# Performance work log

Measured on AMD Instinct MI355X. Metric: run time of the kernel, lower is better.

## Reference

```python
import jax, jax.numpy as jnp
import numpy as np

N_NODES = 100000
N_EDGES = 3200000
DIM = 128
N_LAYERS = 3
NUM_GRAPHS = 128
BN_EPS = 1e-5
GIN_EPS = 0.0  # eps buffer initialized to 0, train_eps=False


def setup_inputs() -> dict:
    key = jax.random.key(0)
    ks = jax.random.split(key, 12)
    s = 1.0 / np.sqrt(DIM)
    inp = {
        "x": jax.random.normal(ks[0], (N_NODES, DIM), jnp.float32),
        "edge_index": jax.random.randint(ks[1], (2, N_EDGES), 0, N_NODES, jnp.int64),
        "batch": jnp.sort(jax.random.randint(ks[2], (N_NODES,), 0, NUM_GRAPHS, jnp.int64)),
        # node encoder Linear(x_dim, emb_dim)
        "W_node": jax.random.uniform(ks[3], (DIM, DIM), jnp.float32, -s, s),
        "b_node": jax.random.uniform(ks[4], (DIM,), jnp.float32, -s, s),
        # per-layer MLP: Linear -> BatchNorm -> ReLU -> Linear, stacked over layers
        "W1": jax.random.uniform(ks[5], (N_LAYERS, DIM, DIM), jnp.float32, -s, s),
        "b1": jax.random.uniform(ks[6], (N_LAYERS, DIM), jnp.float32, -s, s),
        "gamma": jnp.ones((N_LAYERS, DIM), jnp.float32),
        "beta": jnp.zeros((N_LAYERS, DIM), jnp.float32),
        "W2": jax.random.uniform(ks[7], (N_LAYERS, DIM, DIM), jnp.float32, -s, s),
        "b2": jax.random.uniform(ks[8], (N_LAYERS, DIM), jnp.float32, -s, s),
    }
    return inp


def _batchnorm(y, gamma, beta):
    # training-mode batch statistics over the node dimension (biased variance)
    mean = jnp.mean(y, axis=0)
    var = jnp.mean(jnp.square(y - mean), axis=0)
    return (y - mean) * jax.lax.rsqrt(var + BN_EPS) * gamma + beta


def reference(x, edge_index, batch, W_node, b_node, W1, b1, gamma, beta, W2, b2):
    src, dst = edge_index[0], edge_index[1]
    n = x.shape[0]
    h = x @ W_node + b_node  # [N, D]
    for i in range(N_LAYERS):
        # GINConv: scatter-add gathered neighbor features, eps-residual, MLP
        agg = jax.ops.segment_sum(h[src], dst, num_segments=n)  # [N, D]
        out = agg + (1.0 + GIN_EPS) * h
        y = out @ W1[i] + b1[i]
        y = jax.nn.relu(_batchnorm(y, gamma[i], beta[i]))
        y = y @ W2[i] + b2[i]
        h = jax.nn.relu(y)  # outer ReLU in Encoder.forward (dropout_p=0)
    # global_add_pool
    return jax.ops.segment_sum(h, batch, num_segments=NUM_GRAPHS)  # [G, D]
```

## Files before the change

### kernel.cpp

```cpp
#include <hip/hip_runtime.h>

#define N_NODES 100000
#define M_PAD   100096
#define N_EDGES 3200000
#define DIM 128
#define N_LAYERS 3
#define NUM_GRAPHS 128
#define BN_EPS 1e-5f

#define DST_SHIFT 7
#define BUCKET_NODES 128
#define N_BUCKETS ((N_NODES + BUCKET_NODES - 1) / BUCKET_NODES)
#define BUCKET_CAP 4864
#define EDGES_PER_BLOCK 16384
#define BIN_BLOCKS ((N_EDGES + EDGES_PER_BLOCK - 1) / EDGES_PER_BLOCK)
#define N_BANDS 64

typedef unsigned int uint32;
typedef unsigned short u16;
typedef __attribute__((ext_vector_type(8))) short bf16x8;
typedef __attribute__((ext_vector_type(4))) float f32x4;

__device__ __forceinline__ float bf2f(u16 u) {
    union { uint32 i; float f; } c;
    c.i = ((uint32)u) << 16;
    return c.f;
}
__device__ __forceinline__ u16 f2bf(float f) {
    union { float f; uint32 i; } c;
    c.f = f;
    uint32 i = c.i;
    return (u16)((i + 0x7FFFu + ((i >> 16) & 1u)) >> 16);
}
__device__ __forceinline__ float lo_bf(uint32 v) {
    union { uint32 i; float f; } c;
    c.i = v << 16;
    return c.f;
}
__device__ __forceinline__ float hi_bf(uint32 v) {
    union { uint32 i; float f; } c;
    c.i = v & 0xFFFF0000u;
    return c.f;
}
__device__ __forceinline__ uint32 pack_bf2(float a, float b) {
    return ((uint32)f2bf(b) << 16) | (uint32)f2bf(a);
}
__device__ __forceinline__ void unpack_add8(float* acc, uint4 v) {
    acc[0] += lo_bf(v.x); acc[1] += hi_bf(v.x);
    acc[2] += lo_bf(v.y); acc[3] += hi_bf(v.y);
    acc[4] += lo_bf(v.z); acc[5] += hi_bf(v.z);
    acc[6] += lo_bf(v.w); acc[7] += hi_bf(v.w);
}

__global__ __launch_bounds__(256) void zero_misc(int* __restrict__ gcur,
                                                 float* __restrict__ bn_stats,
                                                 float* __restrict__ outp,
                                                 uint32* __restrict__ aggpad32) {
    int i = blockIdx.x * 256 + threadIdx.x;
    if (i < N_BUCKETS) gcur[i] = 0;
    if (i < N_LAYERS * 2 * DIM) bn_stats[i] = 0.f;
    if (i < NUM_GRAPHS * DIM) outp[i] = 0.f;
    if (i < (M_PAD - N_NODES) * DIM / 2) aggpad32[i] = 0;
}

__global__ __launch_bounds__(256) void bin_by_dst(const int* __restrict__ src,
                                                  const int* __restrict__ dst,
                                                  int* __restrict__ gcur,
                                                  uint32* __restrict__ packed) {
    __shared__ int cnt[N_BUCKETS];
    __shared__ int cur[N_BUCKETS];
    int t = threadIdx.x;
    int e0 = blockIdx.x * EDGES_PER_BLOCK;
    for (int i = t; i < N_BUCKETS; i += 256) cnt[i] = 0;
    __syncthreads();

    for (int j = 0; j < EDGES_PER_BLOCK / 256; ++j) {
        int e = e0 + j * 256 + t;
        if (e < N_EDGES) atomicAdd(&cnt[dst[e] >> DST_SHIFT], 1);
    }
    __syncthreads();
    for (int i = t; i < N_BUCKETS; i += 256) {
        int c = cnt[i];
        cur[i] = c ? atomicAdd(&gcur[i], c) : 0;
    }
    __syncthreads();
    for (int j = 0; j < EDGES_PER_BLOCK / 256; ++j) {
        int e = e0 + j * 256 + t;
        if (e < N_EDGES) {
            int d = dst[e];
            int b = d >> DST_SHIFT;
            int pos = atomicAdd(&cur[b], 1);
            if (pos < BUCKET_CAP)
                packed[(size_t)b * BUCKET_CAP + pos] =
                    (uint32)src[e] | ((uint32)(d & (BUCKET_NODES - 1)) << 17);
        }
    }
}

__global__ void scan_buckets(const int* __restrict__ gcur, int* __restrict__ obase,
                             int* __restrict__ row_ptr) {
    __shared__ int s[N_BUCKETS];
    int t = threadIdx.x;
    for (int i = t; i < N_BUCKETS; i += 256) {
        int c = gcur[i];
        s[i] = (c > BUCKET_CAP) ? BUCKET_CAP : c;
    }
    __syncthreads();
    if (t == 0) {
        int run = 0;
        for (int i = 0; i < N_BUCKETS; ++i) {
            int c = s[i];
            s[i] = run;
            run += c;
        }
        row_ptr[N_NODES] = run;
    }
    __syncthreads();
    for (int i = t; i < N_BUCKETS; i += 256) obase[i] = s[i];
}

__global__ __launch_bounds__(256) void build_buckets(const uint32* __restrict__ packed,
                                                     const int* __restrict__ gcur,
                                                     const int* __restrict__ obase_arr,
                                                     int* __restrict__ row_ptr,
                                                     int* __restrict__ col_src) {
    __shared__ uint32 ed[BUCKET_CAP];
    __shared__ uint32 ed2[BUCKET_CAP];
    __shared__ int bandcur[N_BANDS];
    __shared__ int ncnt[BUCKET_NODES];
    __shared__ int ncur[BUCKET_NODES];
    int b = blockIdx.x, t = threadIdx.x;
    int cnt = gcur[b];
    if (cnt > BUCKET_CAP) cnt = BUCKET_CAP;
    int obase = obase_arr[b];
    int n0 = b * BUCKET_NODES;

    if (t < N_BANDS) bandcur[t] = 0;
    if (t < BUCKET_NODES) ncnt[t] = 0;
    __syncthreads();

    const uint32* reg = packed + (size_t)b * BUCKET_CAP;
    for (int i = t; i < cnt; i += 256) {
        uint32 v = reg[i];
        ed[i] = v;
        atomicAdd(&bandcur[(v & 0x1FFFFu) >> 11], 1);
        atomicAdd(&ncnt[v >> 17], 1);
    }
    __syncthreads();

    if (t == 0) {
        int run = 0;
        for (int w = 0; w < N_BANDS; ++w) {
            int c = bandcur[w];
            bandcur[w] = run;
            run += c;
        }
    }
    int myc = (t < BUCKET_NODES) ? ncnt[t] : 0;
    if (t < BUCKET_NODES) ncur[t] = myc;
    __syncthreads();
    for (int off = 1; off < BUCKET_NODES; off <<= 1) {
        int v = 0;
        if (t < BUCKET_NODES && t >= off) v = ncur[t - off];
        __syncthreads();
        if (t < BUCKET_NODES) ncur[t] += v;
        __syncthreads();
    }
    if (t < BUCKET_NODES) {
        int excl = ncur[t] - myc;
        ncur[t] = excl;
        int gn = n0 + t;
        if (gn < N_NODES) row_ptr[gn] = obase + excl;
    }
    __syncthreads();

    for (int i = t; i < cnt; i += 256) {
        uint32 v = ed[i];
        int p = atomicAdd(&bandcur[(v & 0x1FFFFu) >> 11], 1);
        ed2[p] = v;
    }
    __syncthreads();

    for (int i = t; i < cnt; i += 256) {
        uint32 v = ed2[i];
        int slot = atomicAdd(&ncur[v >> 17], 1);
        col_src[obase + slot] = (int)(v & 0x1FFFFu);
    }
}

__global__ void cvt_wt_all(const float* __restrict__ Wn, const float* __restrict__ W1,
                           const float* __restrict__ W2, u16* __restrict__ WT) {
    int m = blockIdx.x >> 7, n = blockIdx.x & 127, k = threadIdx.x;
    const float* src = (m == 0) ? Wn
                     : (m <= 3) ? W1 + (size_t)(m - 1) * DIM * DIM
                                : W2 + (size_t)(m - 4) * DIM * DIM;
    int L = n * 256 + k * 2;
    int Ls = L ^ ((n & 7) << 4);
    *(u16*)((char*)WT + (size_t)m * 32768 + Ls) = f2bf(src[(size_t)k * DIM + n]);
}

__global__ __launch_bounds__(256) void aggregate_bf(const u16* __restrict__ h,
                                                    const int* __restrict__ row_ptr,
                                                    const int* __restrict__ col_src,
                                                    u16* __restrict__ agg) {
    int t = threadIdx.x;
    int quad = (blockIdx.x * 256 + t) >> 4;
    int c = t & 15;
    int nA = quad * 2;
    if (nA >= N_NODES) return;
    int nB = nA + 1;
    const uint4* h4 = (const uint4*)h;

    int begA = row_ptr[nA], endA = row_ptr[nA + 1];
    int begB = row_ptr[nB], endB = row_ptr[nB + 1];
    int lenA = endA - begA, lenB = endB - begB;
    int m = lenA < lenB ? lenA : lenB;

    float a_[8], b_[8];
#pragma unroll
    for (int j = 0; j < 8; ++j) { a_[j] = 0.f; b_[j] = 0.f; }

    {
        uint4 sA = h4[(size_t)nA * 16 + c];
        uint4 sB = h4[(size_t)nB * 16 + c];
        unpack_add8(a_, sA);
        unpack_add8(b_, sB);
    }

    int i = 0;
    for (; i + 2 <= m; i += 2) {
        int iA0 = col_src[begA + i], iA1 = col_src[begA + i + 1];
        int iB0 = col_src[begB + i], iB1 = col_src[begB + i + 1];
        uint4 vA0 = h4[(size_t)iA0 * 16 + c];
        uint4 vB0 = h4[(size_t)iB0 * 16 + c];
        uint4 vA1 = h4[(size_t)iA1 * 16 + c];
        uint4 vB1 = h4[(size_t)iB1 * 16 + c];
        unpack_add8(a_, vA0);
        unpack_add8(b_, vB0);
        unpack_add8(a_, vA1);
        unpack_add8(b_, vB1);
    }
    if (i < m) {
        uint4 vA = h4[(size_t)col_src[begA + i] * 16 + c];
        uint4 vB = h4[(size_t)col_src[begB + i] * 16 + c];
        unpack_add8(a_, vA);
        unpack_add8(b_, vB);
        ++i;
    }
    for (int e = begA + i; e < endA; ++e) {
        uint4 v = h4[(size_t)col_src[e] * 16 + c];
        unpack_add8(a_, v);
    }
    for (int e = begB + i; e < endB; ++e) {
        uint4 v = h4[(size_t)col_src[e] * 16 + c];
        unpack_add8(b_, v);
    }

    uint4 oA, oB;
    oA.x = pack_bf2(a_[0], a_[1]); oA.y = pack_bf2(a_[2], a_[3]);
    oA.z = pack_bf2(a_[4], a_[5]); oA.w = pack_bf2(a_[6], a_[7]);
    oB.x = pack_bf2(b_[0], b_[1]); oB.y = pack_bf2(b_[2], b_[3]);
    oB.z = pack_bf2(b_[4], b_[5]); oB.w = pack_bf2(b_[6], b_[7]);
    *(uint4*)&agg[(size_t)nA * DIM + c * 8] = oA;
    *(uint4*)&agg[(size_t)nB * DIM + c * 8] = oB;
}

template <int MODE>
__global__ __launch_bounds__(256) void gemm_v2(const void* __restrict__ Av,
                                               const u16* __restrict__ WTs,
                                               const float* __restrict__ bias,
                                               u16* __restrict__ outp,
                                               float* __restrict__ bn_sum,
                                               float* __restrict__ bn_sumsq,
                                               const float* __restrict__ gamma,
                                               const float* __restrict__ beta) {
    __shared__ u16 sB[DIM * DIM];
    __shared__ float sc_[DIM];
    __shared__ float sh_[DIM];
    __shared__ float ls[4][DIM];
    __shared__ float lq[4][DIM];

    int t = threadIdx.x;
    int wid = t >> 6, lane = t & 63;
    int hw = lane >> 4, c = lane & 15;
    int row0 = blockIdx.x * 128 + wid * 32;

    bf16x8 a[2][4];
    float4 af[2][4][2];
#pragma unroll
    for (int rf = 0; rf < 2; ++rf) {
        int row = row0 + rf * 16 + c;
#pragma unroll
        for (int ks = 0; ks < 4; ++ks) {
            int k0 = ks * 32 + hw * 8;
            if (MODE == 0) {
                const float* xf = (const float*)Av;
                af[rf][ks][0] = make_float4(0.f, 0.f, 0.f, 0.f);
                af[rf][ks][1] = af[rf][ks][0];
                if (row < N_NODES) {
                    af[rf][ks][0] = *(const float4*)&xf[(size_t)row * DIM + k0];
                    af[rf][ks][1] = *(const float4*)&xf[(size_t)row * DIM + k0 + 4];
                }
            } else {
                const u16* Ab = (const u16*)Av;
                a[rf][ks] = *(const bf16x8*)&Ab[(size_t)row * DIM + k0];
            }
        }
    }

    {
        const uint4* Wg = (const uint4*)WTs;
        uint4* sB4 = (uint4*)sB;
#pragma unroll
        for (int i = 0; i < 8; ++i) sB4[i * 256 + t] = Wg[i * 256 + t];
    }
    if (MODE == 2 && t < DIM) {
        const float invN = 1.0f / (float)N_NODES;
        float mean = bn_sum[t] * invN;
        float var = fmaxf(bn_sumsq[t] * invN - mean * mean, 0.f);
        float rs = rsqrtf(var + BN_EPS);
        float sc = gamma[t] * rs;
        sc_[t] = sc;
        sh_[t] = beta[t] - mean * sc;
    }
    __syncthreads();

#pragma unroll
    for (int rf = 0; rf < 2; ++rf) {
#pragma unroll
        for (int ks = 0; ks < 4; ++ks) {
            int k0 = ks * 32 + hw * 8;
            if (MODE == 0) {
                union { bf16x8 v; u16 u[8]; } ua;
                float4 v0 = af[rf][ks][0], v1 = af[rf][ks][1];
                ua.u[0] = f2bf(v0.x); ua.u[1] = f2bf(v0.y);
                ua.u[2] = f2bf(v0.z); ua.u[3] = f2bf(v0.w);
                ua.u[4] = f2bf(v1.x); ua.u[5] = f2bf(v1.y);
                ua.u[6] = f2bf(v1.z); ua.u[7] = f2bf(v1.w);
                a[rf][ks] = ua.v;
            } else if (MODE == 2) {
                union { bf16x8 v; u16 u[8]; } ua;
                ua.v = a[rf][ks];
#pragma unroll
                for (int j = 0; j < 8; ++j) {
                    float f = bf2f(ua.u[j]);
                    f = fmaxf(fmaf(f, sc_[k0 + j], sh_[k0 + j]), 0.f);
                    ua.u[j] = f2bf(f);
                }
                a[rf][ks] = ua.v;
            }
        }
    }

    f32x4 acc[2][8];
#pragma unroll
    for (int rf = 0; rf < 2; ++rf)
#pragma unroll
        for (int nf = 0; nf < 8; ++nf) acc[rf][nf] = (f32x4){0.f, 0.f, 0.f, 0.f};

    int swz = (c & 7) << 4;
#pragma unroll
    for (int ks = 0; ks < 4; ++ks) {
#pragma unroll
        for (int nf = 0; nf < 8; ++nf) {
            int L = (nf * 4096 + c * 256 + ks * 64 + hw * 16) ^ swz;
            bf16x8 b = *(const bf16x8*)((const char*)sB + L);
            acc[0][nf] = __builtin_amdgcn_mfma_f32_16x16x32_bf16(a[0][ks], b, acc[0][nf], 0, 0, 0);
            acc[1][nf] = __builtin_amdgcn_mfma_f32_16x16x32_bf16(a[1][ks], b, acc[1][nf], 0, 0, 0);
        }
    }

    float s_[8], q_[8];
#pragma unroll
    for (int nf = 0; nf < 8; ++nf) { s_[nf] = 0.f; q_[nf] = 0.f; }

#pragma unroll
    for (int rf = 0; rf < 2; ++rf) {
        int rbase = row0 + rf * 16 + hw * 4;
#pragma unroll
        for (int nf = 0; nf < 8; ++nf) {
            float bv = bias[nf * 16 + c];
#pragma unroll
            for (int r = 0; r < 4; ++r) {
                float v = acc[rf][nf][r] + bv;
                if (MODE == 2) v = fmaxf(v, 0.f);
                outp[(size_t)(rbase + r) * DIM + nf * 16 + c] = f2bf(v);
                if (MODE == 1) {
                    float m = (rbase + r < N_NODES) ? v : 0.f;
                    s_[nf] += m;
                    q_[nf] += m * m;
                }
            }
        }
    }

    if (MODE == 1) {
#pragma unroll
        for (int nf = 0; nf < 8; ++nf) {
            s_[nf] += __shfl_xor(s_[nf], 16);
            s_[nf] += __shfl_xor(s_[nf], 32);
            q_[nf] += __shfl_xor(q_[nf], 16);
            q_[nf] += __shfl_xor(q_[nf], 32);
        }
        if (lane < 16) {
#pragma unroll
            for (int nf = 0; nf < 8; ++nf) {
                ls[wid][nf * 16 + c] = s_[nf];
                lq[wid][nf * 16 + c] = q_[nf];
            }
        }
        __syncthreads();
        if (t < DIM) {
            atomicAdd(&bn_sum[t], ls[0][t] + ls[1][t] + ls[2][t] + ls[3][t]);
            atomicAdd(&bn_sumsq[t], lq[0][t] + lq[1][t] + lq[2][t] + lq[3][t]);
        }
    }
}

__global__ __launch_bounds__(256) void pool_bf(const u16* __restrict__ h,
                                               const int* __restrict__ batch,
                                               float* __restrict__ out) {
    int wv = (blockIdx.x * 256 + threadIdx.x) >> 6;
    int lane = threadIdx.x & 63;
    int base = wv * 32;
    if (base >= N_NODES) return;
    int end = base + 32;
    if (end > N_NODES) end = N_NODES;
    const uint32* h32 = (const uint32*)h;
    float ax = 0.f, ay = 0.f;
    int curg = batch[base];
    for (int n = base; n < end; ++n) {
        int g = batch[n];
        if (g != curg) {
            atomicAdd(&out[curg * DIM + lane * 2], ax);
            atomicAdd(&out[curg * DIM + lane * 2 + 1], ay);
            ax = 0.f;
            ay = 0.f;
            curg = g;
        }
        uint32 v = h32[(size_t)n * 64 + lane];
        ax += lo_bf(v);
        ay += hi_bf(v);
    }
    atomicAdd(&out[curg * DIM + lane * 2], ax);
    atomicAdd(&out[curg * DIM + lane * 2 + 1], ay);
}

extern "C" void kernel_launch(void* const* d_in, const int* in_sizes, int n_in,
                              void* d_out, int out_size, void* d_ws, size_t ws_size,
                              hipStream_t stream) {
    const float* x     = (const float*)d_in[0];
    const int*   ei    = (const int*)d_in[1];
    const int*   batch = (const int*)d_in[2];
    const float* Wn    = (const float*)d_in[3];
    const float* bnode = (const float*)d_in[4];
    const float* W1    = (const float*)d_in[5];
    const float* b1    = (const float*)d_in[6];
    const float* gamma = (const float*)d_in[7];
    const float* beta  = (const float*)d_in[8];
    const float* W2    = (const float*)d_in[9];
    const float* b2    = (const float*)d_in[10];
    float* out = (float*)d_out;

    const int* e_src = ei;
    const int* e_dst = ei + N_EDGES;

    const size_t MD = (size_t)M_PAD * DIM;
    u16* h   = (u16*)d_ws;
    u16* agg = h + MD;
    u16* y   = agg + MD;
    u16* WT  = y + MD;
    int* row_ptr = (int*)(WT + 7 * DIM * DIM);
    int* col_src = row_ptr + N_NODES + 1;
    int* gcur    = col_src + N_EDGES;
    int* obase   = gcur + N_BUCKETS;
    float* bn_stats = (float*)(obase + N_BUCKETS);
    uint32* packed = (uint32*)y;

    const int GEMM_BLOCKS = M_PAD / 128;
    const int AGG_BLOCKS = (N_NODES / 2 * 16 + 255) / 256;
    const int POOL_BLOCKS = (((N_NODES + 31) / 32) * 64 + 255) / 256;

    zero_misc<<<64, 256, 0, stream>>>(gcur, bn_stats, out,
                                      (uint32*)(agg + (size_t)N_NODES * DIM));
    bin_by_dst<<<BIN_BLOCKS, 256, 0, stream>>>(e_src, e_dst, gcur, packed);
    scan_buckets<<<1, 256, 0, stream>>>(gcur, obase, row_ptr);
    build_buckets<<<N_BUCKETS, 256, 0, stream>>>(packed, gcur, obase, row_ptr, col_src);

    cvt_wt_all<<<7 * DIM, DIM, 0, stream>>>(Wn, W1, W2, WT);

    gemm_v2<0><<<GEMM_BLOCKS, 256, 0, stream>>>(x, WT, bnode, h, nullptr,
                                                nullptr, nullptr, nullptr);

    for (int i = 0; i < N_LAYERS; ++i) {
        float* bn_sum = bn_stats + (size_t)i * 2 * DIM;
        float* bn_sumsq = bn_sum + DIM;
        aggregate_bf<<<AGG_BLOCKS, 256, 0, stream>>>(h, row_ptr, col_src, agg);
        gemm_v2<1><<<GEMM_BLOCKS, 256, 0, stream>>>(
            agg, WT + (size_t)(1 + i) * DIM * DIM, b1 + i * DIM, y, bn_sum,
            bn_sumsq, nullptr, nullptr);
        gemm_v2<2><<<GEMM_BLOCKS, 256, 0, stream>>>(
            y, WT + (size_t)(4 + i) * DIM * DIM, b2 + i * DIM, h, bn_sum,
            bn_sumsq, gamma + i * DIM, beta + i * DIM);
    }

    pool_bf<<<POOL_BLOCKS, 256, 0, stream>>>(h, batch, out);
}
```

Before: 653.2 us.

## Store node features in column-block layout and aggregate per column block with degree-sorted nodes

The GEMM epilogues for modes 0 and 2 now write h in a column-blocked layout: eight 16-column slabs, each holding all nodes. The aggregation kernel launches one block group per slab, and each node's 8 lanes gather 32-byte slices, so each pass works over a smaller 3.2MB feature slab that can stay cache-resident. Nodes are processed in an order sorted by in-degree, built by new histogram, scan and scatter kernels, to balance load within waves. The src-band sort in bucket building is dropped, so gather locality within a node's edge list may suffer. Each edge index is now read eight times and each gather is narrower.

```diff
diff --git a/kernel.cpp b/kernel.cpp
--- a/kernel.cpp
+++ b/kernel.cpp
@@ -14,7 +14,6 @@
 #define BUCKET_CAP 4864
 #define EDGES_PER_BLOCK 16384
 #define BIN_BLOCKS ((N_EDGES + EDGES_PER_BLOCK - 1) / EDGES_PER_BLOCK)
-#define N_BANDS 64
 
 typedef unsigned int uint32;
 typedef unsigned short u16;
@@ -45,22 +44,19 @@
 __device__ __forceinline__ uint32 pack_bf2(float a, float b) {
     return ((uint32)f2bf(b) << 16) | (uint32)f2bf(a);
 }
-__device__ __forceinline__ void unpack_add8(float* acc, uint4 v) {
-    acc[0] += lo_bf(v.x); acc[1] += hi_bf(v.x);
-    acc[2] += lo_bf(v.y); acc[3] += hi_bf(v.y);
-    acc[4] += lo_bf(v.z); acc[5] += hi_bf(v.z);
-    acc[6] += lo_bf(v.w); acc[7] += hi_bf(v.w);
-}
+
 
 __global__ __launch_bounds__(256) void zero_misc(int* __restrict__ gcur,
                                                  float* __restrict__ bn_stats,
                                                  float* __restrict__ outp,
-                                                 uint32* __restrict__ aggpad32) {
+                                                 uint32* __restrict__ aggpad32,
+                                                 int* __restrict__ dhist) {
     int i = blockIdx.x * 256 + threadIdx.x;
     if (i < N_BUCKETS) gcur[i] = 0;
     if (i < N_LAYERS * 2 * DIM) bn_stats[i] = 0.f;
     if (i < NUM_GRAPHS * DIM) outp[i] = 0.f;
     if (i < (M_PAD - N_NODES) * DIM / 2) aggpad32[i] = 0;
+    if (i < 256) dhist[i] = 0;
 }
 
 __global__ __launch_bounds__(256) void bin_by_dst(const int* __restrict__ src,
@@ -125,8 +121,6 @@
                                                      int* __restrict__ row_ptr,
                                                      int* __restrict__ col_src) {
     __shared__ uint32 ed[BUCKET_CAP];
-    __shared__ uint32 ed2[BUCKET_CAP];
-    __shared__ int bandcur[N_BANDS];
     __shared__ int ncnt[BUCKET_NODES];
     __shared__ int ncur[BUCKET_NODES];
     int b = blockIdx.x, t = threadIdx.x;
@@ -135,7 +129,6 @@
     int obase = obase_arr[b];
     int n0 = b * BUCKET_NODES;
 
-    if (t < N_BANDS) bandcur[t] = 0;
     if (t < BUCKET_NODES) ncnt[t] = 0;
     __syncthreads();
 
@@ -143,19 +136,10 @@
     for (int i = t; i < cnt; i += 256) {
         uint32 v = reg[i];
         ed[i] = v;
-        atomicAdd(&bandcur[(v & 0x1FFFFu) >> 11], 1);
         atomicAdd(&ncnt[v >> 17], 1);
     }
     __syncthreads();
 
-    if (t == 0) {
-        int run = 0;
-        for (int w = 0; w < N_BANDS; ++w) {
-            int c = bandcur[w];
-            bandcur[w] = run;
-            run += c;
-        }
-    }
     int myc = (t < BUCKET_NODES) ? ncnt[t] : 0;
     if (t < BUCKET_NODES) ncur[t] = myc;
     __syncthreads();
@@ -176,15 +160,45 @@
 
     for (int i = t; i < cnt; i += 256) {
         uint32 v = ed[i];
-        int p = atomicAdd(&bandcur[(v & 0x1FFFFu) >> 11], 1);
-        ed2[p] = v;
-    }
-    __syncthreads();
-
-    for (int i = t; i < cnt; i += 256) {
-        uint32 v = ed2[i];
         int slot = atomicAdd(&ncur[v >> 17], 1);
         col_src[obase + slot] = (int)(v & 0x1FFFFu);
+    }
+}
+
+__global__ __launch_bounds__(256) void deg_hist(const int* __restrict__ row_ptr,
+                                                int* __restrict__ dhist) {
+    int n = blockIdx.x * 256 + threadIdx.x;
+    if (n < N_NODES) {
+        int d = row_ptr[n + 1] - row_ptr[n];
+        if (d > 255) d = 255;
+        atomicAdd(&dhist[d], 1);
+    }
+}
+
+__global__ void deg_scan(const int* __restrict__ dhist, int* __restrict__ dcur) {
+    __shared__ int s[256];
+    int t = threadIdx.x;
+    int my = dhist[t];
+    s[t] = my;
+    __syncthreads();
+    for (int off = 1; off < 256; off <<= 1) {
+        int v = (t >= off) ? s[t - off] : 0;
+        __syncthreads();
+        s[t] += v;
+        __syncthreads();
+    }
+    dcur[t] = s[t] - my;
+}
+
+__global__ __launch_bounds__(256) void deg_scatter(const int* __restrict__ row_ptr,
+                                                   int* __restrict__ dcur,
+                                                   int* __restrict__ perm) {
+    int n = blockIdx.x * 256 + threadIdx.x;
+    if (n < N_NODES) {
+        int d = row_ptr[n + 1] - row_ptr[n];
+        if (d > 255) d = 255;
+        int pos = atomicAdd(&dcur[d], 1);
+        perm[pos] = n;
     }
 }
 
@@ -199,70 +213,41 @@
     *(u16*)((char*)WT + (size_t)m * 32768 + Ls) = f2bf(src[(size_t)k * DIM + n]);
 }
 
-__global__ __launch_bounds__(256) void aggregate_bf(const u16* __restrict__ h,
+__global__ __launch_bounds__(256) void aggregate_cb(const u16* __restrict__ hcb,
                                                     const int* __restrict__ row_ptr,
                                                     const int* __restrict__ col_src,
+                                                    const int* __restrict__ perm,
                                                     u16* __restrict__ agg) {
     int t = threadIdx.x;
-    int quad = (blockIdx.x * 256 + t) >> 4;
-    int c = t & 15;
-    int nA = quad * 2;
-    if (nA >= N_NODES) return;
-    int nB = nA + 1;
-    const uint4* h4 = (const uint4*)h;
-
-    int begA = row_ptr[nA], endA = row_ptr[nA + 1];
-    int begB = row_ptr[nB], endB = row_ptr[nB + 1];
-    int lenA = endA - begA, lenB = endB - begB;
-    int m = lenA < lenB ? lenA : lenB;
-
-    float a_[8], b_[8];
-#pragma unroll
-    for (int j = 0; j < 8; ++j) { a_[j] = 0.f; b_[j] = 0.f; }
-
-    {
-        uint4 sA = h4[(size_t)nA * 16 + c];
-        uint4 sB = h4[(size_t)nB * 16 + c];
-        unpack_add8(a_, sA);
-        unpack_add8(b_, sB);
-    }
-
-    int i = 0;
-    for (; i + 2 <= m; i += 2) {
-        int iA0 = col_src[begA + i], iA1 = col_src[begA + i + 1];
-        int iB0 = col_src[begB + i], iB1 = col_src[begB + i + 1];
-        uint4 vA0 = h4[(size_t)iA0 * 16 + c];
-        uint4 vB0 = h4[(size_t)iB0 * 16 + c];
-        uint4 vA1 = h4[(size_t)iA1 * 16 + c];
-        uint4 vB1 = h4[(size_t)iB1 * 16 + c];
-        unpack_add8(a_, vA0);
-        unpack_add8(b_, vB0);
-        unpack_add8(a_, vA1);
-        unpack_add8(b_, vB1);
-    }
-    if (i < m) {
-        uint4 vA = h4[(size_t)col_src[begA + i] * 16 + c];
-        uint4 vB = h4[(size_t)col_src[begB + i] * 16 + c];
-        unpack_add8(a_, vA);
-        unpack_add8(b_, vB);
-        ++i;
-    }
-    for (int e = begA + i; e < endA; ++e) {
-        uint4 v = h4[(size_t)col_src[e] * 16 + c];
-        unpack_add8(a_, v);
-    }
-    for (int e = begB + i; e < endB; ++e) {
-        uint4 v = h4[(size_t)col_src[e] * 16 + c];
-        unpack_add8(b_, v);
-    }
-
-    uint4 oA, oB;
-    oA.x = pack_bf2(a_[0], a_[1]); oA.y = pack_bf2(a_[2], a_[3]);
-    oA.z = pack_bf2(a_[4], a_[5]); oA.w = pack_bf2(a_[6], a_[7]);
-    oB.x = pack_bf2(b_[0], b_[1]); oB.y = pack_bf2(b_[2], b_[3]);
-    oB.z = pack_bf2(b_[4], b_[5]); oB.w = pack_bf2(b_[6], b_[7]);
-    *(uint4*)&agg[(size_t)nA * DIM + c * 8] = oA;
-    *(uint4*)&agg[(size_t)nB * DIM + c * 8] = oB;
+    int cb = blockIdx.x & 7;
+    int idx = (blockIdx.x >> 3) * 32 + (t >> 3);
+    int l = t & 7;
+    if (idx >= N_NODES) return;
+    int n = perm[idx];
+    const uint32* base = (const uint32*)hcb + (size_t)cb * M_PAD * 8;
+    int beg = row_ptr[n], end = row_ptr[n + 1];
+
+    uint32 sv = base[(size_t)n * 8 + l];
+    float ax = lo_bf(sv), ay = hi_bf(sv);
+
+    int e = beg;
+    for (; e + 3 < end; e += 4) {
+        int s0 = col_src[e], s1 = col_src[e + 1];
+        int s2 = col_src[e + 2], s3 = col_src[e + 3];
+        uint32 v0 = base[(size_t)s0 * 8 + l];
+        uint32 v1 = base[(size_t)s1 * 8 + l];
+        uint32 v2 = base[(size_t)s2 * 8 + l];
+        uint32 v3 = base[(size_t)s3 * 8 + l];
+        ax += lo_bf(v0); ay += hi_bf(v0);
+        ax += lo_bf(v1); ay += hi_bf(v1);
+        ax += lo_bf(v2); ay += hi_bf(v2);
+        ax += lo_bf(v3); ay += hi_bf(v3);
+    }
+    for (; e < end; ++e) {
+        uint32 v = base[(size_t)col_src[e] * 8 + l];
+        ax += lo_bf(v); ay += hi_bf(v);
+    }
+    ((uint32*)agg)[(size_t)n * 64 + cb * 8 + l] = pack_bf2(ax, ay);
 }
 
 template <int MODE>
@@ -384,11 +369,14 @@
             for (int r = 0; r < 4; ++r) {
                 float v = acc[rf][nf][r] + bv;
                 if (MODE == 2) v = fmaxf(v, 0.f);
-                outp[(size_t)(rbase + r) * DIM + nf * 16 + c] = f2bf(v);
+                u16 o = f2bf(v);
                 if (MODE == 1) {
+                    outp[(size_t)(rbase + r) * DIM + nf * 16 + c] = o;
                     float m = (rbase + r < N_NODES) ? v : 0.f;
                     s_[nf] += m;
                     q_[nf] += m * m;
+                } else {
+                    outp[((size_t)nf * M_PAD + (rbase + r)) * 16 + c] = o;
                 }
             }
         }
@@ -417,33 +405,35 @@
     }
 }
 
-__global__ __launch_bounds__(256) void pool_bf(const u16* __restrict__ h,
+__global__ __launch_bounds__(256) void pool_cb(const u16* __restrict__ hcb,
                                                const int* __restrict__ batch,
                                                float* __restrict__ out) {
     int wv = (blockIdx.x * 256 + threadIdx.x) >> 6;
     int lane = threadIdx.x & 63;
+    int cb = lane >> 3, l = lane & 7;
     int base = wv * 32;
     if (base >= N_NODES) return;
     int end = base + 32;
     if (end > N_NODES) end = N_NODES;
-    const uint32* h32 = (const uint32*)h;
+    const uint32* b32 = (const uint32*)hcb + (size_t)cb * M_PAD * 8;
+    int col = cb * 16 + l * 2;
     float ax = 0.f, ay = 0.f;
     int curg = batch[base];
     for (int n = base; n < end; ++n) {
         int g = batch[n];
         if (g != curg) {
-            atomicAdd(&out[curg * DIM + lane * 2], ax);
-            atomicAdd(&out[curg * DIM + lane * 2 + 1], ay);
+            atomicAdd(&out[curg * DIM + col], ax);
+            atomicAdd(&out[curg * DIM + col + 1], ay);
             ax = 0.f;
             ay = 0.f;
             curg = g;
         }
-        uint32 v = h32[(size_t)n * 64 + lane];
+        uint32 v = b32[(size_t)n * 8 + l];
         ax += lo_bf(v);
         ay += hi_bf(v);
     }
-    atomicAdd(&out[curg * DIM + lane * 2], ax);
-    atomicAdd(&out[curg * DIM + lane * 2 + 1], ay);
+    atomicAdd(&out[curg * DIM + col], ax);
+    atomicAdd(&out[curg * DIM + col + 1], ay);
 }
 
 extern "C" void kernel_launch(void* const* d_in, const int* in_sizes, int n_in,
@@ -474,19 +464,27 @@
     int* col_src = row_ptr + N_NODES + 1;
     int* gcur    = col_src + N_EDGES;
     int* obase   = gcur + N_BUCKETS;
-    float* bn_stats = (float*)(obase + N_BUCKETS);
+    int* dhist   = obase + N_BUCKETS;
+    int* dcur    = dhist + 256;
+    int* perm    = dcur + 256;
+    float* bn_stats = (float*)(perm + N_NODES);
     uint32* packed = (uint32*)y;
 
     const int GEMM_BLOCKS = M_PAD / 128;
-    const int AGG_BLOCKS = (N_NODES / 2 * 16 + 255) / 256;
+    const int AGG_BLOCKS = ((N_NODES + 31) / 32) * 8;
     const int POOL_BLOCKS = (((N_NODES + 31) / 32) * 64 + 255) / 256;
+    const int NODE_BLOCKS = (N_NODES + 255) / 256;
 
     zero_misc<<<64, 256, 0, stream>>>(gcur, bn_stats, out,
-                                      (uint32*)(agg + (size_t)N_NODES * DIM));
+                                      (uint32*)(agg + (size_t)N_NODES * DIM), dhist);
     bin_by_dst<<<BIN_BLOCKS, 256, 0, stream>>>(e_src, e_dst, gcur, packed);
     scan_buckets<<<1, 256, 0, stream>>>(gcur, obase, row_ptr);
     build_buckets<<<N_BUCKETS, 256, 0, stream>>>(packed, gcur, obase, row_ptr, col_src);
 
+    deg_hist<<<NODE_BLOCKS, 256, 0, stream>>>(row_ptr, dhist);
+    deg_scan<<<1, 256, 0, stream>>>(dhist, dcur);
+    deg_scatter<<<NODE_BLOCKS, 256, 0, stream>>>(row_ptr, dcur, perm);
+
     cvt_wt_all<<<7 * DIM, DIM, 0, stream>>>(Wn, W1, W2, WT);
 
     gemm_v2<0><<<GEMM_BLOCKS, 256, 0, stream>>>(x, WT, bnode, h, nullptr,
@@ -495,7 +493,7 @@
     for (int i = 0; i < N_LAYERS; ++i) {
         float* bn_sum = bn_stats + (size_t)i * 2 * DIM;
         float* bn_sumsq = bn_sum + DIM;
-        aggregate_bf<<<AGG_BLOCKS, 256, 0, stream>>>(h, row_ptr, col_src, agg);
+        aggregate_cb<<<AGG_BLOCKS, 256, 0, stream>>>(h, row_ptr, col_src, perm, agg);
         gemm_v2<1><<<GEMM_BLOCKS, 256, 0, stream>>>(
             agg, WT + (size_t)(1 + i) * DIM * DIM, b1 + i * DIM, y, bn_sum,
             bn_sumsq, nullptr, nullptr);
@@ -504,5 +502,5 @@
             bn_sumsq, gamma + i * DIM, beta + i * DIM);
     }
 
-    pool_bf<<<POOL_BLOCKS, 256, 0, stream>>>(h, batch, out);
-}
+    pool_cb<<<POOL_BLOCKS, 256, 0, stream>>>(h, batch, out);
+}
```

Result: slower. 1.303 ms (+99.5%).
